# Kernel tuning notes

Measured on AMD Instinct MI355X. Metric: run time of the kernel, lower is better.

Reference implementation:

```python
import jax, jax.numpy as jnp
import numpy as np

STEPS = 10          # points in t_grid -> STEPS-1 RK4 intervals
TRACE_STEPS = 2     # Hutchinson probes per dynamics eval
T_FINAL = 1.0
CLAMP = 100.0


def odefun(t, z, W1, b1, tw1, W2, b2):
    # time-conditioned 2-layer tanh MLP (canonical FFJORD dynamics)
    h = jnp.tanh(z @ W1 + b1 + t * tw1)
    return h @ W2 + b2


def setup_inputs() -> dict:
    key = jax.random.key(0)
    B, D, H = 2048, 512, 1024
    ks = jax.random.split(key, 4)
    s1 = 1.0 / np.sqrt(D)
    s2 = 1.0 / np.sqrt(H)
    return {
        "x": jax.random.normal(ks[0], (B, D), jnp.float32),
        "W1": jax.random.normal(ks[1], (D, H), jnp.float32) * s1,
        "b1": jnp.zeros((H,), jnp.float32),
        "tw1": jax.random.normal(ks[2], (H,), jnp.float32) * 0.1,
        "W2": jax.random.normal(ks[3], (H, D), jnp.float32) * s2,
        "b2": jnp.zeros((D,), jnp.float32),
    }


def reference(x, W1, b1, tw1, W2, b2):
    params = (W1, b1, tw1, W2, b2)
    B, D = x.shape

    def divergence_estimate(t, z, e):
        # torch detaches z before the grad call -> stop_gradient here
        z_sg = jax.lax.stop_gradient(z)
        f, vjp_fn = jax.vjp(lambda zz: odefun(t, zz, *params), z_sg)
        etf = vjp_fn(e)[0]                      # e^T J  (Hutchinson probe)
        return f, jnp.sum(etf * e, axis=-1)     # [B]

    def augmented_dynamics(t, state, key):
        z = state[:, :-1]                        # [B, D]
        div_est = jnp.zeros((B,), state.dtype)
        f_z = None
        for i in range(TRACE_STEPS):             # small fixed loop
            e = jax.random.randint(jax.random.fold_in(key, i), z.shape, 0, 2).astype(z.dtype) * 2.0 - 1.0
            f_z, div = divergence_estimate(t, z, e)
            div_est = div_est + div
        div_est = jnp.clip(div_est / TRACE_STEPS, -CLAMP, CLAMP)
        return jnp.concatenate([f_z, -div_est[:, None]], axis=-1)

    t_grid = jnp.linspace(0.0, T_FINAL, STEPS)
    state0 = jnp.concatenate([x, jnp.zeros((B, 1), x.dtype)], axis=-1)  # [B, D+1]

    def step(carry, t01):
        state, key = carry
        t0, t1 = t01[0], t01[1]
        dt = t1 - t0
        key, k1k, k2k, k3k, k4k = jax.random.split(key, 5)
        # torchdiffeq 'rk4' = Kutta's 3/8-rule variant (rk4_alt_step_func)
        k1 = augmented_dynamics(t0, state, k1k)
        k2 = augmented_dynamics(t0 + dt / 3.0, state + dt * k1 / 3.0, k2k)
        k3 = augmented_dynamics(t0 + dt * 2.0 / 3.0, state + dt * (k2 - k1 / 3.0), k3k)
        k4 = augmented_dynamics(t1, state + dt * (k1 - k2 + k3), k4k)
        state = state + (k1 + 3.0 * (k2 + k3) + k4) * dt * 0.125
        return (state, key), None

    t_pairs = jnp.stack([t_grid[:-1], t_grid[1:]], axis=-1)  # [STEPS-1, 2]
    (state, _), _ = jax.lax.scan(step, (state0, jax.random.key(1234)), t_pairs)

    rep, probsolve = state[:, :-1], state[:, -1]
    logprob = -0.5 * jnp.sum(rep * rep, axis=-1) + probsolve
    return rep, logprob
```

## Files before the change

kernel.cpp:

```cpp
#include <hip/hip_runtime.h>
#include <stdint.h>


#define B_N 2048
#define D_N 512
#define H_N 1024
#define BD (B_N * D_N)

typedef unsigned short u16;
typedef __attribute__((ext_vector_type(8))) short s16x8;
typedef __attribute__((ext_vector_type(4))) float f32x4;

typedef __attribute__((address_space(1))) const uint32_t ga_u32;
typedef __attribute__((address_space(3))) uint32_t ls_u32;

#if __has_builtin(__builtin_amdgcn_alignbit)
#define ROTL32(x, r) __builtin_amdgcn_alignbit((x), (x), 32 - (r))
#else
#define ROTL32(x, r) (((x) << (r)) | ((x) >> (32 - (r))))
#endif

__device__ __forceinline__ u16 f2bf(float f) {
  union { float f; uint32_t u; } c; c.f = f;
  uint32_t r = c.u + 0x7FFFu + ((c.u >> 16) & 1u);
  return (u16)(r >> 16);
}
__device__ __forceinline__ float fast_tanh(float v) {
  float e = __expf(2.0f * fabsf(v));
  float t = 1.0f - 2.0f / (e + 1.0f);
  return copysignf(t, v);
}

struct U2 { uint32_t x, y; };

__device__ __forceinline__ U2 tf2x32(uint32_t k0, uint32_t k1, uint32_t x0, uint32_t x1) {
  uint32_t k2 = k0 ^ k1 ^ 0x1BD11BDAu;
#define RND(r) { x0 += x1; x1 = ROTL32(x1, r); x1 ^= x0; }
  x0 += k0; x1 += k1;
  RND(13) RND(15) RND(26) RND(6)
  x0 += k1; x1 += k2 + 1u;
  RND(17) RND(29) RND(16) RND(24)
  x0 += k2; x1 += k0 + 2u;
  RND(13) RND(15) RND(26) RND(6)
  x0 += k0; x1 += k1 + 3u;
  RND(17) RND(29) RND(16) RND(24)
  x0 += k1; x1 += k2 + 4u;
  RND(13) RND(15) RND(26) RND(6)
  x0 += k2; x1 += k0 + 5u;
#undef RND
  U2 r; r.x = x0; r.y = x1; return r;
}

__global__ void k_keysched(uint32_t* __restrict__ ekeys) {
  if (threadIdx.x != 0 || blockIdx.x != 0) return;
  uint32_t kx = 0u, ky = 1234u;
  for (int s = 0; s < 9; ++s) {
    for (int st = 0; st < 4; ++st) {
      U2 kst = tf2x32(kx, ky, 0u, (uint32_t)(st + 1));
      for (int pr = 0; pr < 2; ++pr) {
        U2 fo = tf2x32(kst.x, kst.y, 0u, (uint32_t)pr);
        U2 k2 = tf2x32(fo.x, fo.y, 0u, 1u);
        ekeys[(s * 4 + st) * 4 + pr * 2 + 0] = k2.x;
        ekeys[(s * 4 + st) * 4 + pr * 2 + 1] = k2.y;
      }
    }
    U2 c = tf2x32(kx, ky, 0u, 0u);
    kx = c.x; ky = c.y;
  }
}

__global__ void k_egen(u16* __restrict__ ebf, const uint32_t* __restrict__ keys, int gs) {
  const int xcd = blockIdx.x & 7, bi = blockIdx.x >> 3;
  const int u = bi * 256 + threadIdx.x;
  const int slab = xcd * 4 + (u >> 13);
  const int r13 = u & 8191;
  const int stage = gs + (r13 >> 11);
  const int r11 = r13 & 2047;
  const int probe = r11 >> 10;
  const int unit = r11 & 1023;
  const uint32_t p0 = (uint32_t)(slab * 32768 + unit * 32);
  uint32_t k0 = keys[stage * 4 + probe * 2], k1 = keys[stage * 4 + probe * 2 + 1];
  uint4* dst = (uint4*)(ebf + (size_t)(stage & 3) * (2 * (size_t)BD) + (size_t)probe * BD + (size_t)p0);
#pragma unroll
  for (int g = 0; g < 4; ++g) {
    uint32_t pr[4];
#pragma unroll
    for (int h = 0; h < 4; ++h) {
      uint32_t c0 = p0 + g * 8 + h * 2;
      U2 r0 = tf2x32(k0, k1, 0u, c0);
      U2 r1 = tf2x32(k0, k1, 0u, c0 + 1u);
      pr[h] = (((r0.x ^ r0.y) & 1u) ? 0x3F80u : 0xBF80u) |
              (((r1.x ^ r1.y) & 1u) ? 0x3F800000u : 0xBF800000u);
    }
    uint4 v; v.x = pr[0]; v.y = pr[1]; v.z = pr[2]; v.w = pr[3];
    dst[g] = v;
  }
}

__global__ void k_init(const float* __restrict__ x, float* __restrict__ z, u16* __restrict__ zin,
                       float* __restrict__ lp, float* __restrict__ d0, float* __restrict__ d1) {
  int i = blockIdx.x * 256 + threadIdx.x;
  if (i < BD) { float v = x[i]; z[i] = v; zin[i] = f2bf(v); }
  if (i < B_N) { lp[i] = 0.f; d0[i] = 0.f; d1[i] = 0.f; }
}

__global__ void k_cvtT(const float* __restrict__ src, u16* __restrict__ dst, int R, int C) {
  int i = blockIdx.x * 256 + threadIdx.x;
  if (i >= R * C) return;
  int c = i / R, r = i - c * R;
  dst[i] = f2bf(src[(size_t)r * C + c]);
}
__global__ void k_cvt(const float* __restrict__ src, u16* __restrict__ dst, int n) {
  int i = blockIdx.x * 256 + threadIdx.x;
  if (i < n) dst[i] = f2bf(src[i]);
}

__global__ void k_sentinel(float* __restrict__ out, int n) {
  int i = blockIdx.x * 256 + threadIdx.x;
  if (i < n) out[i] = 12345.0f;
}


__global__ __launch_bounds__(256)
void k_f1(const u16* __restrict__ zin, const u16* __restrict__ e0g, const u16* __restrict__ e1g,
          const u16* __restrict__ W1T, const u16* __restrict__ W2b,
          const float* __restrict__ b1v, const float* __restrict__ tw1v, float tstage,
          u16* __restrict__ hbuf, float* __restrict__ div0, float* __restrict__ div1) {
  __shared__ u16 S[2][5 * 2048];
  const int tid = threadIdx.x, wave = tid >> 6, lane = tid & 63;
  const int xcd = blockIdx.x & 7, idx = blockIdx.x >> 3;
  const int bm = xcd * 4 + (idx >> 4);
  const int bh = idx & 15;
  const int row0 = bm * 64, col0 = bh * 64;
  const int wm = wave >> 1, wn = wave & 1, r16 = lane & 15, q = lane >> 4;
  const int srow = lane >> 2;
  const int scol = (((lane & 3) ^ ((srow >> 1) & 3))) * 8;
  const int cqa = (q ^ ((r16 >> 1) & 3)) * 8;

  f32x4 az[2][2], au0[2][2], au1[2][2], av0[2][2], av1[2][2];
#pragma unroll
  for (int i = 0; i < 2; ++i)
#pragma unroll
    for (int j = 0; j < 2; ++j) {
      az[i][j] = (f32x4){0,0,0,0}; au0[i][j] = (f32x4){0,0,0,0}; au1[i][j] = (f32x4){0,0,0,0};
      av0[i][j] = (f32x4){0,0,0,0}; av1[i][j] = (f32x4){0,0,0,0};
    }

  const size_t arow = (size_t)(row0 + wave * 16 + srow) * 512 + scol;
  const size_t brow = (size_t)(col0 + wave * 16 + srow) * 512 + scol;
  auto stage = [&](int kt, int buf) {
    u16* b = &S[buf][0];
    __builtin_amdgcn_global_load_lds((ga_u32*)(zin + arow + kt), (ls_u32*)(b + 0    + wave * 512), 16, 0, 0);
    __builtin_amdgcn_global_load_lds((ga_u32*)(e0g + arow + kt), (ls_u32*)(b + 2048 + wave * 512), 16, 0, 0);
    __builtin_amdgcn_global_load_lds((ga_u32*)(e1g + arow + kt), (ls_u32*)(b + 4096 + wave * 512), 16, 0, 0);
    __builtin_amdgcn_global_load_lds((ga_u32*)(W1T + brow + kt), (ls_u32*)(b + 6144 + wave * 512), 16, 0, 0);
    __builtin_amdgcn_global_load_lds((ga_u32*)(W2b + brow + kt), (ls_u32*)(b + 8192 + wave * 512), 16, 0, 0);
  };
  stage(0, 0);
  for (int it = 0; it < 16; ++it) {
    const int buf = it & 1;
    __syncthreads();
    if (it + 1 < 16) stage((it + 1) * 32, buf ^ 1);
    const u16* b = &S[buf][0];
    s16x8 zf[2], e0f[2], e1f[2], w1f[2], w2f[2];
#pragma unroll
    for (int i = 0; i < 2; ++i) {
      const int ao = (wm * 32 + i * 16 + r16) * 32 + cqa;
      zf[i]  = *(const s16x8*)(b + 0    + ao);
      e0f[i] = *(const s16x8*)(b + 2048 + ao);
      e1f[i] = *(const s16x8*)(b + 4096 + ao);
    }
#pragma unroll
    for (int j = 0; j < 2; ++j) {
      const int bo = (wn * 32 + j * 16 + r16) * 32 + cqa;
      w1f[j] = *(const s16x8*)(b + 6144 + bo);
      w2f[j] = *(const s16x8*)(b + 8192 + bo);
    }
#pragma unroll
    for (int i = 0; i < 2; ++i)
#pragma unroll
      for (int j = 0; j < 2; ++j) {
        az[i][j]  = __builtin_amdgcn_mfma_f32_16x16x32_bf16(zf[i],  w1f[j], az[i][j],  0, 0, 0);
        au0[i][j] = __builtin_amdgcn_mfma_f32_16x16x32_bf16(e0f[i], w1f[j], au0[i][j], 0, 0, 0);
        au1[i][j] = __builtin_amdgcn_mfma_f32_16x16x32_bf16(e1f[i], w1f[j], au1[i][j], 0, 0, 0);
        av0[i][j] = __builtin_amdgcn_mfma_f32_16x16x32_bf16(e0f[i], w2f[j], av0[i][j], 0, 0, 0);
        av1[i][j] = __builtin_amdgcn_mfma_f32_16x16x32_bf16(e1f[i], w2f[j], av1[i][j], 0, 0, 0);
      }
  }

  float d0s[2][4], d1s[2][4];
#pragma unroll
  for (int i = 0; i < 2; ++i)
#pragma unroll
    for (int r = 0; r < 4; ++r) { d0s[i][r] = 0.f; d1s[i][r] = 0.f; }

#pragma unroll
  for (int j = 0; j < 2; ++j) {
    const int gcol = col0 + wn * 32 + j * 16 + r16;
    const float colb = b1v[gcol] + tstage * tw1v[gcol];
#pragma unroll
    for (int i = 0; i < 2; ++i) {
      const int rbase = row0 + wm * 32 + i * 16 + q * 4;
#pragma unroll
      for (int r = 0; r < 4; ++r) {
        float hv = fast_tanh(az[i][j][r] + colb);
        hbuf[(size_t)(rbase + r) * H_N + gcol] = f2bf(hv);
        float s = 1.f - hv * hv;
        d0s[i][r] += s * au0[i][j][r] * av0[i][j][r];
        d1s[i][r] += s * au1[i][j][r] * av1[i][j][r];
      }
    }
  }
#pragma unroll
  for (int i = 0; i < 2; ++i)
#pragma unroll
    for (int r = 0; r < 4; ++r) {
      float a = d0s[i][r], bb = d1s[i][r];
#pragma unroll
      for (int m = 1; m < 16; m <<= 1) { a += __shfl_xor(a, m); bb += __shfl_xor(bb, m); }
      if (r16 == 0) {
        int grow = row0 + wm * 32 + i * 16 + q * 4 + r;
        atomicAdd(&div0[grow], a);
        atomicAdd(&div1[grow], bb);
      }
    }
}

template<int ST>
__global__ __launch_bounds__(256)
void k_f3(const u16* __restrict__ hbuf, const u16* __restrict__ W2T, const float* __restrict__ b2v,
          float* __restrict__ z, float* __restrict__ ACC, float* __restrict__ T,
          u16* __restrict__ zin, float dt,
          float* __restrict__ lp, float* __restrict__ div0, float* __restrict__ div1, float wdt) {
  __shared__ u16 S[2][3 * 2048];
  const int tid = threadIdx.x, wave = tid >> 6, lane = tid & 63;
  const int xcd = blockIdx.x & 7, idx = blockIdx.x >> 3;
  const int bm = xcd * 4 + (idx >> 4);
  const int bn = idx & 15;
  const int row0 = bm * 64, col0 = bn * 32;
  const int r16 = lane & 15, q = lane >> 4;
  const int srow = lane >> 2;
  const int scol = (((lane & 3) ^ ((srow >> 1) & 3))) * 8;
  const int cqa = (q ^ ((r16 >> 1) & 3)) * 8;

  if (bn == 0 && tid < 64) {
    int b = row0 + tid;
    float c = 0.5f * (div0[b] + div1[b]);
    c = fminf(fmaxf(c, -100.f), 100.f);
    lp[b] -= wdt * c;
    div0[b] = 0.f; div1[b] = 0.f;
  }

  f32x4 acc[2];
  acc[0] = (f32x4){0,0,0,0}; acc[1] = (f32x4){0,0,0,0};

  const size_t arow = (size_t)(row0 + wave * 16 + srow) * 1024 + scol;
  const size_t brow = (size_t)(col0 + (wave & 1) * 16 + srow) * 1024 + scol;
  auto stage = [&](int kt, int buf) {
    u16* b = &S[buf][0];
    __builtin_amdgcn_global_load_lds((ga_u32*)(hbuf + arow + kt), (ls_u32*)(b + wave * 512), 16, 0, 0);
    if (wave < 2)
      __builtin_amdgcn_global_load_lds((ga_u32*)(W2T + brow + kt), (ls_u32*)(b + 4096 + wave * 512), 16, 0, 0);
  };
  stage(0, 0);
  for (int it = 0; it < 32; ++it) {
    const int buf = it & 1;
    __syncthreads();
    if (it + 1 < 32) stage((it + 1) * 32, buf ^ 1);
    const u16* b = &S[buf][0];
    s16x8 af  = *(const s16x8*)(b + (wave * 16 + r16) * 32 + cqa);
    s16x8 bf0 = *(const s16x8*)(b + 4096 + r16 * 32 + cqa);
    s16x8 bf1 = *(const s16x8*)(b + 4096 + (16 + r16) * 32 + cqa);
    acc[0] = __builtin_amdgcn_mfma_f32_16x16x32_bf16(af, bf0, acc[0], 0, 0, 0);
    acc[1] = __builtin_amdgcn_mfma_f32_16x16x32_bf16(af, bf1, acc[1], 0, 0, 0);
  }

#pragma unroll
  for (int j = 0; j < 2; ++j) {
    const int gcol = col0 + j * 16 + r16;
    const float cb = b2v[gcol];
    const int rbase = row0 + wave * 16 + q * 4;
#pragma unroll
    for (int r = 0; r < 4; ++r) {
      const size_t idx2 = (size_t)(rbase + r) * D_N + gcol;
      const float f = acc[j][r] + cb;
      if (ST == 0) {
        ACC[idx2] = dt * 0.125f * f;
        T[idx2]   = dt * f;
        zin[idx2] = f2bf(z[idx2] + dt * f * (1.f / 3.f));
      } else if (ST == 1) {
        float t_ = T[idx2];
        ACC[idx2] += 0.375f * dt * f;
        zin[idx2] = f2bf(z[idx2] + dt * f - t_ * (1.f / 3.f));
        T[idx2]   = t_ - dt * f;
      } else if (ST == 2) {
        ACC[idx2] += 0.375f * dt * f;
        zin[idx2] = f2bf(z[idx2] + T[idx2] + dt * f);
      } else {
        float zn = z[idx2] + ACC[idx2] + dt * 0.125f * f;
        z[idx2]   = zn;
        zin[idx2] = f2bf(zn);
      }
    }
  }
}

__global__ void k_out(const float* __restrict__ z, const float* __restrict__ lp,
                      float* __restrict__ out) {
  const int xcd = blockIdx.x & 7, idx = blockIdx.x >> 3;
  const int b = (xcd * 4 + (idx >> 6)) * 64 + (idx & 63);
  int t = threadIdx.x;
  const float* zr = z + (size_t)b * D_N;
  float ss = 0.f;
  for (int d = t; d < D_N; d += 256) {
    float v = zr[d];
    out[(size_t)b * D_N + d] = v;
    ss += v * v;
  }
  for (int off = 32; off > 0; off >>= 1) ss += __shfl_down(ss, off);
  __shared__ float red[4];
  if ((t & 63) == 0) red[t >> 6] = ss;
  __syncthreads();
  if (t == 0) out[(size_t)BD + b] = -0.5f * (red[0] + red[1] + red[2] + red[3]) + lp[b];
}

extern "C" void kernel_launch(void* const* d_in, const int* in_sizes, int n_in,
                              void* d_out, int out_size, void* d_ws, size_t ws_size,
                              hipStream_t stream) {
  const float* x   = (const float*)d_in[0];
  const float* W1  = (const float*)d_in[1];
  const float* b1  = (const float*)d_in[2];
  const float* tw1 = (const float*)d_in[3];
  const float* W2  = (const float*)d_in[4];
  const float* b2  = (const float*)d_in[5];
  float* outp = (float*)d_out;

  const size_t NEEDED = (size_t)45 << 20;
  if (ws_size < NEEDED) {
    k_sentinel<<<(BD + B_N + 255) / 256, 256, 0, stream>>>(outp, BD + B_N);
    return;
  }
  char* w = (char*)d_ws;
  auto carve = [&](size_t bytes) { char* p = w; w += (bytes + 255) & ~(size_t)255; return p; };
  uint32_t* keys = (uint32_t*)carve(144 * sizeof(uint32_t));
  u16* ebf   = (u16*)carve((size_t)4 * 2 * BD * 2);
  float* z   = (float*)carve((size_t)BD * 4);
  float* ACC = (float*)carve((size_t)BD * 4);
  float* T   = (float*)carve((size_t)BD * 4);
  u16* zin   = (u16*)carve((size_t)BD * 2);
  u16* hbuf  = (u16*)carve((size_t)B_N * H_N * 2);
  u16* W1T   = (u16*)carve((size_t)H_N * D_N * 2);
  u16* W2b   = (u16*)carve((size_t)H_N * D_N * 2);
  u16* W2T   = (u16*)carve((size_t)D_N * H_N * 2);
  float* lp   = (float*)carve((size_t)B_N * 4);
  float* div0 = (float*)carve((size_t)B_N * 4);
  float* div1 = (float*)carve((size_t)B_N * 4);

  k_keysched<<<1, 1, 0, stream>>>(keys);
  k_init<<<BD / 256, 256, 0, stream>>>(x, z, zin, lp, div0, div1);
  k_cvtT<<<(D_N * H_N) / 256, 256, 0, stream>>>(W1, W1T, D_N, H_N);
  k_cvt <<<(H_N * D_N) / 256, 256, 0, stream>>>(W2, W2b, H_N * D_N);
  k_cvtT<<<(H_N * D_N) / 256, 256, 0, stream>>>(W2, W2T, H_N, D_N);

  const int gF1 = (B_N / 64) * (H_N / 64);
  const int gF3 = (B_N / 64) * (D_N / 32);

  for (int s = 0; s < 9; ++s) {
    float t0 = (float)s / 9.0f;
    float t1 = (float)(s + 1) / 9.0f;
    float dt = t1 - t0;
    float tst[4] = { t0, t0 + dt / 3.0f, t0 + dt * 2.0f / 3.0f, t1 };
    float wts[4] = { 1.f, 3.f, 3.f, 1.f };
    for (int st = 0; st < 4; ++st) {
      const int sg = s * 4 + st;
      if ((sg & 3) == 0) k_egen<<<1024, 256, 0, stream>>>(ebf, keys, sg);
      const u16* e0g = ebf + (size_t)(sg & 3) * (2 * (size_t)BD);
      const u16* e1g = e0g + BD;
      k_f1<<<gF1, 256, 0, stream>>>(zin, e0g, e1g, W1T, W2b, b1, tw1, tst[st], hbuf, div0, div1);
      const float wdt = dt * 0.125f * wts[st];
      if (st == 0)      k_f3<0><<<gF3, 256, 0, stream>>>(hbuf, W2T, b2, z, ACC, T, zin, dt, lp, div0, div1, wdt);
      else if (st == 1) k_f3<1><<<gF3, 256, 0, stream>>>(hbuf, W2T, b2, z, ACC, T, zin, dt, lp, div0, div1, wdt);
      else if (st == 2) k_f3<2><<<gF3, 256, 0, stream>>>(hbuf, W2T, b2, z, ACC, T, zin, dt, lp, div0, div1, wdt);
      else              k_f3<3><<<gF3, 256, 0, stream>>>(hbuf, W2T, b2, z, ACC, T, zin, dt, lp, div0, div1, wdt);
    }
  }
  k_out<<<B_N, 256, 0, stream>>>(z, lp, outp);
}
```

Measured before the change: 1.401 ms.

## Load A operands directly to registers and enlarge f3 tiles to 64x64

In k_f1 the z/e0/e1 activation fragments are now read straight from global memory into registers with a double-buffered register prefetch. Only the W1T/W2 tiles still go through LDS, so shared memory drops from five tiles to two. k_f3 moves from 64x32 to 64x64 output tiles with a 2x2 wave layout, halving its grid, and also loads hbuf fragments directly into registers. Both kernels get launch_bounds with a minimum of 2 blocks per CU, and the k-loops are fully unrolled. The aim is to cut LDS traffic and reuse each B fragment across more rows, at the cost of uncoalesced 16-byte direct global loads and more register pressure.

```diff
diff --git a/kernel.cpp b/kernel.cpp
--- a/kernel.cpp
+++ b/kernel.cpp
@@ -120,13 +120,12 @@
   if (i < n) out[i] = 12345.0f;
 }
 
-
-__global__ __launch_bounds__(256)
+__global__ __launch_bounds__(256, 2)
 void k_f1(const u16* __restrict__ zin, const u16* __restrict__ e0g, const u16* __restrict__ e1g,
           const u16* __restrict__ W1T, const u16* __restrict__ W2b,
           const float* __restrict__ b1v, const float* __restrict__ tw1v, float tstage,
           u16* __restrict__ hbuf, float* __restrict__ div0, float* __restrict__ div1) {
-  __shared__ u16 S[2][5 * 2048];
+  __shared__ u16 S[2][2 * 2048];
   const int tid = threadIdx.x, wave = tid >> 6, lane = tid & 63;
   const int xcd = blockIdx.x & 7, idx = blockIdx.x >> 3;
   const int bm = xcd * 4 + (idx >> 4);
@@ -146,45 +145,47 @@
       av0[i][j] = (f32x4){0,0,0,0}; av1[i][j] = (f32x4){0,0,0,0};
     }
 
-  const size_t arow = (size_t)(row0 + wave * 16 + srow) * 512 + scol;
+  const size_t a0 = (size_t)(row0 + wm * 32 + r16) * 512 + q * 8;
+  const size_t a1 = a0 + (size_t)16 * 512;
   const size_t brow = (size_t)(col0 + wave * 16 + srow) * 512 + scol;
-  auto stage = [&](int kt, int buf) {
+  auto stageB = [&](int kt, int buf) {
     u16* b = &S[buf][0];
-    __builtin_amdgcn_global_load_lds((ga_u32*)(zin + arow + kt), (ls_u32*)(b + 0    + wave * 512), 16, 0, 0);
-    __builtin_amdgcn_global_load_lds((ga_u32*)(e0g + arow + kt), (ls_u32*)(b + 2048 + wave * 512), 16, 0, 0);
-    __builtin_amdgcn_global_load_lds((ga_u32*)(e1g + arow + kt), (ls_u32*)(b + 4096 + wave * 512), 16, 0, 0);
-    __builtin_amdgcn_global_load_lds((ga_u32*)(W1T + brow + kt), (ls_u32*)(b + 6144 + wave * 512), 16, 0, 0);
-    __builtin_amdgcn_global_load_lds((ga_u32*)(W2b + brow + kt), (ls_u32*)(b + 8192 + wave * 512), 16, 0, 0);
+    __builtin_amdgcn_global_load_lds((ga_u32*)(W1T + brow + kt), (ls_u32*)(b + 0    + wave * 512), 16, 0, 0);
+    __builtin_amdgcn_global_load_lds((ga_u32*)(W2b + brow + kt), (ls_u32*)(b + 2048 + wave * 512), 16, 0, 0);
   };
-  stage(0, 0);
+  s16x8 A[2][6];
+  auto aload = [&](int kt, int slot) {
+    A[slot][0] = *(const s16x8*)(zin + a0 + kt);
+    A[slot][1] = *(const s16x8*)(zin + a1 + kt);
+    A[slot][2] = *(const s16x8*)(e0g + a0 + kt);
+    A[slot][3] = *(const s16x8*)(e0g + a1 + kt);
+    A[slot][4] = *(const s16x8*)(e1g + a0 + kt);
+    A[slot][5] = *(const s16x8*)(e1g + a1 + kt);
+  };
+  stageB(0, 0);
+  aload(0, 0);
+#pragma unroll
   for (int it = 0; it < 16; ++it) {
     const int buf = it & 1;
     __syncthreads();
-    if (it + 1 < 16) stage((it + 1) * 32, buf ^ 1);
+    if (it + 1 < 16) { stageB((it + 1) * 32, buf ^ 1); aload((it + 1) * 32, buf ^ 1); }
     const u16* b = &S[buf][0];
-    s16x8 zf[2], e0f[2], e1f[2], w1f[2], w2f[2];
-#pragma unroll
-    for (int i = 0; i < 2; ++i) {
-      const int ao = (wm * 32 + i * 16 + r16) * 32 + cqa;
-      zf[i]  = *(const s16x8*)(b + 0    + ao);
-      e0f[i] = *(const s16x8*)(b + 2048 + ao);
-      e1f[i] = *(const s16x8*)(b + 4096 + ao);
-    }
+    s16x8 w1f[2], w2f[2];
 #pragma unroll
     for (int j = 0; j < 2; ++j) {
       const int bo = (wn * 32 + j * 16 + r16) * 32 + cqa;
-      w1f[j] = *(const s16x8*)(b + 6144 + bo);
-      w2f[j] = *(const s16x8*)(b + 8192 + bo);
+      w1f[j] = *(const s16x8*)(b + 0    + bo);
+      w2f[j] = *(const s16x8*)(b + 2048 + bo);
     }
 #pragma unroll
     for (int i = 0; i < 2; ++i)
 #pragma unroll
       for (int j = 0; j < 2; ++j) {
-        az[i][j]  = __builtin_amdgcn_mfma_f32_16x16x32_bf16(zf[i],  w1f[j], az[i][j],  0, 0, 0);
-        au0[i][j] = __builtin_amdgcn_mfma_f32_16x16x32_bf16(e0f[i], w1f[j], au0[i][j], 0, 0, 0);
-        au1[i][j] = __builtin_amdgcn_mfma_f32_16x16x32_bf16(e1f[i], w1f[j], au1[i][j], 0, 0, 0);
-        av0[i][j] = __builtin_amdgcn_mfma_f32_16x16x32_bf16(e0f[i], w2f[j], av0[i][j], 0, 0, 0);
-        av1[i][j] = __builtin_amdgcn_mfma_f32_16x16x32_bf16(e1f[i], w2f[j], av1[i][j], 0, 0, 0);
+        az[i][j]  = __builtin_amdgcn_mfma_f32_16x16x32_bf16(A[buf][i],     w1f[j], az[i][j],  0, 0, 0);
+        au0[i][j] = __builtin_amdgcn_mfma_f32_16x16x32_bf16(A[buf][2 + i], w1f[j], au0[i][j], 0, 0, 0);
+        au1[i][j] = __builtin_amdgcn_mfma_f32_16x16x32_bf16(A[buf][4 + i], w1f[j], au1[i][j], 0, 0, 0);
+        av0[i][j] = __builtin_amdgcn_mfma_f32_16x16x32_bf16(A[buf][2 + i], w2f[j], av0[i][j], 0, 0, 0);
+        av1[i][j] = __builtin_amdgcn_mfma_f32_16x16x32_bf16(A[buf][4 + i], w2f[j], av1[i][j], 0, 0, 0);
       }
   }
 
@@ -227,18 +228,18 @@
 }
 
 template<int ST>
-__global__ __launch_bounds__(256)
+__global__ __launch_bounds__(256, 2)
 void k_f3(const u16* __restrict__ hbuf, const u16* __restrict__ W2T, const float* __restrict__ b2v,
           float* __restrict__ z, float* __restrict__ ACC, float* __restrict__ T,
           u16* __restrict__ zin, float dt,
           float* __restrict__ lp, float* __restrict__ div0, float* __restrict__ div1, float wdt) {
-  __shared__ u16 S[2][3 * 2048];
+  __shared__ u16 S[2][2048];
   const int tid = threadIdx.x, wave = tid >> 6, lane = tid & 63;
   const int xcd = blockIdx.x & 7, idx = blockIdx.x >> 3;
-  const int bm = xcd * 4 + (idx >> 4);
-  const int bn = idx & 15;
-  const int row0 = bm * 64, col0 = bn * 32;
-  const int r16 = lane & 15, q = lane >> 4;
+  const int bm = xcd * 4 + (idx >> 3);
+  const int bn = idx & 7;
+  const int row0 = bm * 64, col0 = bn * 64;
+  const int wm = wave >> 1, wn = wave & 1, r16 = lane & 15, q = lane >> 4;
   const int srow = lane >> 2;
   const int scol = (((lane & 3) ^ ((srow >> 1) & 3))) * 8;
   const int cqa = (q ^ ((r16 >> 1) & 3)) * 8;
@@ -251,55 +252,70 @@
     div0[b] = 0.f; div1[b] = 0.f;
   }
 
-  f32x4 acc[2];
-  acc[0] = (f32x4){0,0,0,0}; acc[1] = (f32x4){0,0,0,0};
-
-  const size_t arow = (size_t)(row0 + wave * 16 + srow) * 1024 + scol;
-  const size_t brow = (size_t)(col0 + (wave & 1) * 16 + srow) * 1024 + scol;
-  auto stage = [&](int kt, int buf) {
-    u16* b = &S[buf][0];
-    __builtin_amdgcn_global_load_lds((ga_u32*)(hbuf + arow + kt), (ls_u32*)(b + wave * 512), 16, 0, 0);
-    if (wave < 2)
-      __builtin_amdgcn_global_load_lds((ga_u32*)(W2T + brow + kt), (ls_u32*)(b + 4096 + wave * 512), 16, 0, 0);
+  f32x4 acc[2][2];
+#pragma unroll
+  for (int i = 0; i < 2; ++i)
+#pragma unroll
+    for (int j = 0; j < 2; ++j) acc[i][j] = (f32x4){0,0,0,0};
+
+  const size_t a0 = (size_t)(row0 + wm * 32 + r16) * 1024 + q * 8;
+  const size_t a1 = a0 + (size_t)16 * 1024;
+  const size_t brow = (size_t)(col0 + wave * 16 + srow) * 1024 + scol;
+  auto stageB = [&](int kt, int buf) {
+    __builtin_amdgcn_global_load_lds((ga_u32*)(W2T + brow + kt), (ls_u32*)(&S[buf][0] + wave * 512), 16, 0, 0);
   };
-  stage(0, 0);
+  s16x8 A[2][2];
+  auto aload = [&](int kt, int slot) {
+    A[slot][0] = *(const s16x8*)(hbuf + a0 + kt);
+    A[slot][1] = *(const s16x8*)(hbuf + a1 + kt);
+  };
+  stageB(0, 0);
+  aload(0, 0);
+#pragma unroll
   for (int it = 0; it < 32; ++it) {
     const int buf = it & 1;
     __syncthreads();
-    if (it + 1 < 32) stage((it + 1) * 32, buf ^ 1);
+    if (it + 1 < 32) { stageB((it + 1) * 32, buf ^ 1); aload((it + 1) * 32, buf ^ 1); }
     const u16* b = &S[buf][0];
-    s16x8 af  = *(const s16x8*)(b + (wave * 16 + r16) * 32 + cqa);
-    s16x8 bf0 = *(const s16x8*)(b + 4096 + r16 * 32 + cqa);
-    s16x8 bf1 = *(const s16x8*)(b + 4096 + (16 + r16) * 32 + cqa);
-    acc[0] = __builtin_amdgcn_mfma_f32_16x16x32_bf16(af, bf0, acc[0], 0, 0, 0);
-    acc[1] = __builtin_amdgcn_mfma_f32_16x16x32_bf16(af, bf1, acc[1], 0, 0, 0);
+    s16x8 bfr[2];
+#pragma unroll
+    for (int j = 0; j < 2; ++j)
+      bfr[j] = *(const s16x8*)(b + (wn * 32 + j * 16 + r16) * 32 + cqa);
+#pragma unroll
+    for (int i = 0; i < 2; ++i)
+#pragma unroll
+      for (int j = 0; j < 2; ++j)
+        acc[i][j] = __builtin_amdgcn_mfma_f32_16x16x32_bf16(A[buf][i], bfr[j], acc[i][j], 0, 0, 0);
   }
 
 #pragma unroll
   for (int j = 0; j < 2; ++j) {
-    const int gcol = col0 + j * 16 + r16;
+    const int gcol = col0 + wn * 32 + j * 16 + r16;
     const float cb = b2v[gcol];
-    const int rbase = row0 + wave * 16 + q * 4;
-#pragma unroll
-    for (int r = 0; r < 4; ++r) {
-      const size_t idx2 = (size_t)(rbase + r) * D_N + gcol;
-      const float f = acc[j][r] + cb;
-      if (ST == 0) {
-        ACC[idx2] = dt * 0.125f * f;
-        T[idx2]   = dt * f;
-        zin[idx2] = f2bf(z[idx2] + dt * f * (1.f / 3.f));
-      } else if (ST == 1) {
-        float t_ = T[idx2];
-        ACC[idx2] += 0.375f * dt * f;
-        zin[idx2] = f2bf(z[idx2] + dt * f - t_ * (1.f / 3.f));
-        T[idx2]   = t_ - dt * f;
-      } else if (ST == 2) {
-        ACC[idx2] += 0.375f * dt * f;
-        zin[idx2] = f2bf(z[idx2] + T[idx2] + dt * f);
-      } else {
-        float zn = z[idx2] + ACC[idx2] + dt * 0.125f * f;
-        z[idx2]   = zn;
-        zin[idx2] = f2bf(zn);
+#pragma unroll
+    for (int i = 0; i < 2; ++i) {
+      const int rbase = row0 + wm * 32 + i * 16 + q * 4;
+#pragma unroll
+      for (int r = 0; r < 4; ++r) {
+        const size_t idx2 = (size_t)(rbase + r) * D_N + gcol;
+        const float f = acc[i][j][r] + cb;
+        if (ST == 0) {
+          ACC[idx2] = dt * 0.125f * f;
+          T[idx2]   = dt * f;
+          zin[idx2] = f2bf(z[idx2] + dt * f * (1.f / 3.f));
+        } else if (ST == 1) {
+          float t_ = T[idx2];
+          ACC[idx2] += 0.375f * dt * f;
+          zin[idx2] = f2bf(z[idx2] + dt * f - t_ * (1.f / 3.f));
+          T[idx2]   = t_ - dt * f;
+        } else if (ST == 2) {
+          ACC[idx2] += 0.375f * dt * f;
+          zin[idx2] = f2bf(z[idx2] + T[idx2] + dt * f);
+        } else {
+          float zn = z[idx2] + ACC[idx2] + dt * 0.125f * f;
+          z[idx2]   = zn;
+          zin[idx2] = f2bf(zn);
+        }
       }
     }
   }
@@ -363,7 +379,7 @@
   k_cvtT<<<(H_N * D_N) / 256, 256, 0, stream>>>(W2, W2T, H_N, D_N);
 
   const int gF1 = (B_N / 64) * (H_N / 64);
-  const int gF3 = (B_N / 64) * (D_N / 32);
+  const int gF3 = (B_N / 64) * (D_N / 64);
 
   for (int s = 0; s < 9; ++s) {
     float t0 = (float)s / 9.0f;
```

Result: slower. 2.084 ms (+48.7%).

## Fuse next-stage probe generation into k_f3 epilogue and widen k_f1 to 8 waves

Applied to the files above, without the earlier changes.

Removes the separate k_egen launch that generated probe vectors for four stages at once. k_f3 now generates the Rademacher probes for the next stage in its epilogue into a double buffer, and a small kernel seeds the first stage. k_f1 runs with 512 threads, so each wave owns a 16-row slice instead of 32, with the LDS staging loop distributed across 8 waves. The intent is to cut launch count, shrink the workspace, and raise occupancy in the first GEMM, at the cost of extra per-block RNG work in k_f3 and less register reuse per wave in k_f1.

```diff
diff --git a/kernel.cpp b/kernel.cpp
--- a/kernel.cpp
+++ b/kernel.cpp
@@ -69,18 +69,12 @@
   }
 }
 
-__global__ void k_egen(u16* __restrict__ ebf, const uint32_t* __restrict__ keys, int gs) {
-  const int xcd = blockIdx.x & 7, bi = blockIdx.x >> 3;
-  const int u = bi * 256 + threadIdx.x;
-  const int slab = xcd * 4 + (u >> 13);
-  const int r13 = u & 8191;
-  const int stage = gs + (r13 >> 11);
-  const int r11 = r13 & 2047;
-  const int probe = r11 >> 10;
-  const int unit = r11 & 1023;
-  const uint32_t p0 = (uint32_t)(slab * 32768 + unit * 32);
-  uint32_t k0 = keys[stage * 4 + probe * 2], k1 = keys[stage * 4 + probe * 2 + 1];
-  uint4* dst = (uint4*)(ebf + (size_t)(stage & 3) * (2 * (size_t)BD) + (size_t)probe * BD + (size_t)p0);
+__global__ void k_egen1(u16* __restrict__ ebf, const uint32_t* __restrict__ keys) {
+  int t = blockIdx.x * 256 + threadIdx.x;
+  int probe = t >> 15, idx = t & 32767;
+  uint32_t p0 = (uint32_t)idx * 32;
+  uint32_t k0 = keys[probe * 2], k1 = keys[probe * 2 + 1];
+  uint4* dst = (uint4*)(ebf + (size_t)probe * BD + (size_t)p0);
 #pragma unroll
   for (int g = 0; g < 4; ++g) {
     uint32_t pr[4];
@@ -120,8 +114,7 @@
   if (i < n) out[i] = 12345.0f;
 }
 
-
-__global__ __launch_bounds__(256)
+__global__ __launch_bounds__(512, 4)
 void k_f1(const u16* __restrict__ zin, const u16* __restrict__ e0g, const u16* __restrict__ e1g,
           const u16* __restrict__ W1T, const u16* __restrict__ W2b,
           const float* __restrict__ b1v, const float* __restrict__ tw1v, float tstage,
@@ -137,24 +130,21 @@
   const int scol = (((lane & 3) ^ ((srow >> 1) & 3))) * 8;
   const int cqa = (q ^ ((r16 >> 1) & 3)) * 8;
 
-  f32x4 az[2][2], au0[2][2], au1[2][2], av0[2][2], av1[2][2];
-#pragma unroll
-  for (int i = 0; i < 2; ++i)
-#pragma unroll
-    for (int j = 0; j < 2; ++j) {
-      az[i][j] = (f32x4){0,0,0,0}; au0[i][j] = (f32x4){0,0,0,0}; au1[i][j] = (f32x4){0,0,0,0};
-      av0[i][j] = (f32x4){0,0,0,0}; av1[i][j] = (f32x4){0,0,0,0};
-    }
-
-  const size_t arow = (size_t)(row0 + wave * 16 + srow) * 512 + scol;
-  const size_t brow = (size_t)(col0 + wave * 16 + srow) * 512 + scol;
+  f32x4 az[2], au0[2], au1[2], av0[2], av1[2];
+#pragma unroll
+  for (int j = 0; j < 2; ++j) {
+    az[j] = (f32x4){0,0,0,0}; au0[j] = (f32x4){0,0,0,0}; au1[j] = (f32x4){0,0,0,0};
+    av0[j] = (f32x4){0,0,0,0}; av1[j] = (f32x4){0,0,0,0};
+  }
+
   auto stage = [&](int kt, int buf) {
     u16* b = &S[buf][0];
-    __builtin_amdgcn_global_load_lds((ga_u32*)(zin + arow + kt), (ls_u32*)(b + 0    + wave * 512), 16, 0, 0);
-    __builtin_amdgcn_global_load_lds((ga_u32*)(e0g + arow + kt), (ls_u32*)(b + 2048 + wave * 512), 16, 0, 0);
-    __builtin_amdgcn_global_load_lds((ga_u32*)(e1g + arow + kt), (ls_u32*)(b + 4096 + wave * 512), 16, 0, 0);
-    __builtin_amdgcn_global_load_lds((ga_u32*)(W1T + brow + kt), (ls_u32*)(b + 6144 + wave * 512), 16, 0, 0);
-    __builtin_amdgcn_global_load_lds((ga_u32*)(W2b + brow + kt), (ls_u32*)(b + 8192 + wave * 512), 16, 0, 0);
+    for (int c = wave; c < 20; c += 8) {
+      const int arr = c >> 2, ch = c & 3;
+      const size_t off = (size_t)((arr < 3 ? row0 : col0) + ch * 16 + srow) * 512 + kt + scol;
+      const u16* src = (arr == 0 ? zin : arr == 1 ? e0g : arr == 2 ? e1g : arr == 3 ? W1T : W2b) + off;
+      __builtin_amdgcn_global_load_lds((ga_u32*)src, (ls_u32*)(b + arr * 2048 + ch * 512), 16, 0, 0);
+    }
   };
   stage(0, 0);
   for (int it = 0; it < 16; ++it) {
@@ -162,14 +152,11 @@
     __syncthreads();
     if (it + 1 < 16) stage((it + 1) * 32, buf ^ 1);
     const u16* b = &S[buf][0];
-    s16x8 zf[2], e0f[2], e1f[2], w1f[2], w2f[2];
-#pragma unroll
-    for (int i = 0; i < 2; ++i) {
-      const int ao = (wm * 32 + i * 16 + r16) * 32 + cqa;
-      zf[i]  = *(const s16x8*)(b + 0    + ao);
-      e0f[i] = *(const s16x8*)(b + 2048 + ao);
-      e1f[i] = *(const s16x8*)(b + 4096 + ao);
-    }
+    const int ao = (wm * 16 + r16) * 32 + cqa;
+    s16x8 zf  = *(const s16x8*)(b + 0    + ao);
+    s16x8 e0f = *(const s16x8*)(b + 2048 + ao);
+    s16x8 e1f = *(const s16x8*)(b + 4096 + ao);
+    s16x8 w1f[2], w2f[2];
 #pragma unroll
     for (int j = 0; j < 2; ++j) {
       const int bo = (wn * 32 + j * 16 + r16) * 32 + cqa;
@@ -177,53 +164,43 @@
       w2f[j] = *(const s16x8*)(b + 8192 + bo);
     }
 #pragma unroll
-    for (int i = 0; i < 2; ++i)
-#pragma unroll
-      for (int j = 0; j < 2; ++j) {
-        az[i][j]  = __builtin_amdgcn_mfma_f32_16x16x32_bf16(zf[i],  w1f[j], az[i][j],  0, 0, 0);
-        au0[i][j] = __builtin_amdgcn_mfma_f32_16x16x32_bf16(e0f[i], w1f[j], au0[i][j], 0, 0, 0);
-        au1[i][j] = __builtin_amdgcn_mfma_f32_16x16x32_bf16(e1f[i], w1f[j], au1[i][j], 0, 0, 0);
-        av0[i][j] = __builtin_amdgcn_mfma_f32_16x16x32_bf16(e0f[i], w2f[j], av0[i][j], 0, 0, 0);
-        av1[i][j] = __builtin_amdgcn_mfma_f32_16x16x32_bf16(e1f[i], w2f[j], av1[i][j], 0, 0, 0);
-      }
-  }
-
-  float d0s[2][4], d1s[2][4];
-#pragma unroll
-  for (int i = 0; i < 2; ++i)
-#pragma unroll
-    for (int r = 0; r < 4; ++r) { d0s[i][r] = 0.f; d1s[i][r] = 0.f; }
-
+    for (int j = 0; j < 2; ++j) {
+      az[j]  = __builtin_amdgcn_mfma_f32_16x16x32_bf16(zf,  w1f[j], az[j],  0, 0, 0);
+      au0[j] = __builtin_amdgcn_mfma_f32_16x16x32_bf16(e0f, w1f[j], au0[j], 0, 0, 0);
+      au1[j] = __builtin_amdgcn_mfma_f32_16x16x32_bf16(e1f, w1f[j], au1[j], 0, 0, 0);
+      av0[j] = __builtin_amdgcn_mfma_f32_16x16x32_bf16(e0f, w2f[j], av0[j], 0, 0, 0);
+      av1[j] = __builtin_amdgcn_mfma_f32_16x16x32_bf16(e1f, w2f[j], av1[j], 0, 0, 0);
+    }
+  }
+
+  float d0s[4], d1s[4];
+#pragma unroll
+  for (int r = 0; r < 4; ++r) { d0s[r] = 0.f; d1s[r] = 0.f; }
+
+  const int rbase = row0 + wm * 16 + q * 4;
 #pragma unroll
   for (int j = 0; j < 2; ++j) {
     const int gcol = col0 + wn * 32 + j * 16 + r16;
     const float colb = b1v[gcol] + tstage * tw1v[gcol];
 #pragma unroll
-    for (int i = 0; i < 2; ++i) {
-      const int rbase = row0 + wm * 32 + i * 16 + q * 4;
-#pragma unroll
-      for (int r = 0; r < 4; ++r) {
-        float hv = fast_tanh(az[i][j][r] + colb);
-        hbuf[(size_t)(rbase + r) * H_N + gcol] = f2bf(hv);
-        float s = 1.f - hv * hv;
-        d0s[i][r] += s * au0[i][j][r] * av0[i][j][r];
-        d1s[i][r] += s * au1[i][j][r] * av1[i][j][r];
-      }
-    }
-  }
-#pragma unroll
-  for (int i = 0; i < 2; ++i)
-#pragma unroll
     for (int r = 0; r < 4; ++r) {
-      float a = d0s[i][r], bb = d1s[i][r];
-#pragma unroll
-      for (int m = 1; m < 16; m <<= 1) { a += __shfl_xor(a, m); bb += __shfl_xor(bb, m); }
-      if (r16 == 0) {
-        int grow = row0 + wm * 32 + i * 16 + q * 4 + r;
-        atomicAdd(&div0[grow], a);
-        atomicAdd(&div1[grow], bb);
-      }
-    }
+      float hv = fast_tanh(az[j][r] + colb);
+      hbuf[(size_t)(rbase + r) * H_N + gcol] = f2bf(hv);
+      float s = 1.f - hv * hv;
+      d0s[r] += s * au0[j][r] * av0[j][r];
+      d1s[r] += s * au1[j][r] * av1[j][r];
+    }
+  }
+#pragma unroll
+  for (int r = 0; r < 4; ++r) {
+    float a = d0s[r], bb = d1s[r];
+#pragma unroll
+    for (int m = 1; m < 16; m <<= 1) { a += __shfl_xor(a, m); bb += __shfl_xor(bb, m); }
+    if (r16 == 0) {
+      atomicAdd(&div0[rbase + r], a);
+      atomicAdd(&div1[rbase + r], bb);
+    }
+  }
 }
 
 template<int ST>
@@ -231,7 +208,8 @@
 void k_f3(const u16* __restrict__ hbuf, const u16* __restrict__ W2T, const float* __restrict__ b2v,
           float* __restrict__ z, float* __restrict__ ACC, float* __restrict__ T,
           u16* __restrict__ zin, float dt,
-          float* __restrict__ lp, float* __restrict__ div0, float* __restrict__ div1, float wdt) {
+          float* __restrict__ lp, float* __restrict__ div0, float* __restrict__ div1, float wdt,
+          const uint32_t* __restrict__ keys, int sg, u16* __restrict__ ebfnext) {
   __shared__ u16 S[2][3 * 2048];
   const int tid = threadIdx.x, wave = tid >> 6, lane = tid & 63;
   const int xcd = blockIdx.x & 7, idx = blockIdx.x >> 3;
@@ -303,6 +281,27 @@
       }
     }
   }
+
+  if (ebfnext) {
+    const int pr = tid >> 7, u = tid & 127;
+    const uint32_t p0 = (uint32_t)(bm * 32768 + bn * 2048 + u * 16);
+    const uint32_t k0 = keys[(sg + 1) * 4 + pr * 2], k1 = keys[(sg + 1) * 4 + pr * 2 + 1];
+    uint4* dst = (uint4*)(ebfnext + (size_t)pr * BD + (size_t)p0);
+#pragma unroll
+    for (int g = 0; g < 2; ++g) {
+      uint32_t pk[4];
+#pragma unroll
+      for (int h = 0; h < 4; ++h) {
+        uint32_t c0 = p0 + g * 8 + h * 2;
+        U2 r0 = tf2x32(k0, k1, 0u, c0);
+        U2 r1 = tf2x32(k0, k1, 0u, c0 + 1u);
+        pk[h] = (((r0.x ^ r0.y) & 1u) ? 0x3F80u : 0xBF80u) |
+                (((r1.x ^ r1.y) & 1u) ? 0x3F800000u : 0xBF800000u);
+      }
+      uint4 v; v.x = pk[0]; v.y = pk[1]; v.z = pk[2]; v.w = pk[3];
+      dst[g] = v;
+    }
+  }
 }
 
 __global__ void k_out(const float* __restrict__ z, const float* __restrict__ lp,
@@ -335,7 +334,7 @@
   const float* b2  = (const float*)d_in[5];
   float* outp = (float*)d_out;
 
-  const size_t NEEDED = (size_t)45 << 20;
+  const size_t NEEDED = (size_t)40 << 20;
   if (ws_size < NEEDED) {
     k_sentinel<<<(BD + B_N + 255) / 256, 256, 0, stream>>>(outp, BD + B_N);
     return;
@@ -343,7 +342,7 @@
   char* w = (char*)d_ws;
   auto carve = [&](size_t bytes) { char* p = w; w += (bytes + 255) & ~(size_t)255; return p; };
   uint32_t* keys = (uint32_t*)carve(144 * sizeof(uint32_t));
-  u16* ebf   = (u16*)carve((size_t)4 * 2 * BD * 2);
+  u16* ebf   = (u16*)carve((size_t)2 * 2 * BD * 2);
   float* z   = (float*)carve((size_t)BD * 4);
   float* ACC = (float*)carve((size_t)BD * 4);
   float* T   = (float*)carve((size_t)BD * 4);
@@ -357,6 +356,7 @@
   float* div1 = (float*)carve((size_t)B_N * 4);
 
   k_keysched<<<1, 1, 0, stream>>>(keys);
+  k_egen1<<<256, 256, 0, stream>>>(ebf, keys);
   k_init<<<BD / 256, 256, 0, stream>>>(x, z, zin, lp, div0, div1);
   k_cvtT<<<(D_N * H_N) / 256, 256, 0, stream>>>(W1, W1T, D_N, H_N);
   k_cvt <<<(H_N * D_N) / 256, 256, 0, stream>>>(W2, W2b, H_N * D_N);
@@ -373,15 +373,15 @@
     float wts[4] = { 1.f, 3.f, 3.f, 1.f };
     for (int st = 0; st < 4; ++st) {
       const int sg = s * 4 + st;
-      if ((sg & 3) == 0) k_egen<<<1024, 256, 0, stream>>>(ebf, keys, sg);
-      const u16* e0g = ebf + (size_t)(sg & 3) * (2 * (size_t)BD);
+      const u16* e0g = ebf + (size_t)(sg & 1) * (2 * (size_t)BD);
       const u16* e1g = e0g + BD;
-      k_f1<<<gF1, 256, 0, stream>>>(zin, e0g, e1g, W1T, W2b, b1, tw1, tst[st], hbuf, div0, div1);
+      u16* enext = (sg + 1 < 36) ? ebf + (size_t)((sg + 1) & 1) * (2 * (size_t)BD) : nullptr;
+      k_f1<<<gF1, 512, 0, stream>>>(zin, e0g, e1g, W1T, W2b, b1, tw1, tst[st], hbuf, div0, div1);
       const float wdt = dt * 0.125f * wts[st];
-      if (st == 0)      k_f3<0><<<gF3, 256, 0, stream>>>(hbuf, W2T, b2, z, ACC, T, zin, dt, lp, div0, div1, wdt);
-      else if (st == 1) k_f3<1><<<gF3, 256, 0, stream>>>(hbuf, W2T, b2, z, ACC, T, zin, dt, lp, div0, div1, wdt);
-      else if (st == 2) k_f3<2><<<gF3, 256, 0, stream>>>(hbuf, W2T, b2, z, ACC, T, zin, dt, lp, div0, div1, wdt);
-      else              k_f3<3><<<gF3, 256, 0, stream>>>(hbuf, W2T, b2, z, ACC, T, zin, dt, lp, div0, div1, wdt);
+      if (st == 0)      k_f3<0><<<gF3, 256, 0, stream>>>(hbuf, W2T, b2, z, ACC, T, zin, dt, lp, div0, div1, wdt, keys, sg, enext);
+      else if (st == 1) k_f3<1><<<gF3, 256, 0, stream>>>(hbuf, W2T, b2, z, ACC, T, zin, dt, lp, div0, div1, wdt, keys, sg, enext);
+      else if (st == 2) k_f3<2><<<gF3, 256, 0, stream>>>(hbuf, W2T, b2, z, ACC, T, zin, dt, lp, div0, div1, wdt, keys, sg, enext);
+      else              k_f3<3><<<gF3, 256, 0, stream>>>(hbuf, W2T, b2, z, ACC, T, zin, dt, lp, div0, div1, wdt, keys, sg, enext);
     }
   }
   k_out<<<B_N, 256, 0, stream>>>(z, lp, outp);
```

Measured after the change: 1.502 ms. 7.2% more time.

## Bit-pack Rademacher probes and generate next-stage bits inside the f3 epilogue

Applied to the files above, without the earlier changes.

Probe vectors are stored as one bit per element instead of bf16 tiles and are expanded into MFMA operands in registers inside k_f1. The LDS staging drops from five arrays to three. The separate k_egen launch is removed: the next stage's probe bits are computed in the k_f3 epilogue and double-buffered. This targets the global and LDS traffic for the probes and one kernel launch per RK step, at the cost of extra ALU work for expansion and threefry hashing in the f3 tail.

```diff
diff --git a/kernel.cpp b/kernel.cpp
--- a/kernel.cpp
+++ b/kernel.cpp
@@ -69,32 +69,18 @@
   }
 }
 
-__global__ void k_egen(u16* __restrict__ ebf, const uint32_t* __restrict__ keys, int gs) {
-  const int xcd = blockIdx.x & 7, bi = blockIdx.x >> 3;
-  const int u = bi * 256 + threadIdx.x;
-  const int slab = xcd * 4 + (u >> 13);
-  const int r13 = u & 8191;
-  const int stage = gs + (r13 >> 11);
-  const int r11 = r13 & 2047;
-  const int probe = r11 >> 10;
-  const int unit = r11 & 1023;
-  const uint32_t p0 = (uint32_t)(slab * 32768 + unit * 32);
-  uint32_t k0 = keys[stage * 4 + probe * 2], k1 = keys[stage * 4 + probe * 2 + 1];
-  uint4* dst = (uint4*)(ebf + (size_t)(stage & 3) * (2 * (size_t)BD) + (size_t)probe * BD + (size_t)p0);
-#pragma unroll
-  for (int g = 0; g < 4; ++g) {
-    uint32_t pr[4];
-#pragma unroll
-    for (int h = 0; h < 4; ++h) {
-      uint32_t c0 = p0 + g * 8 + h * 2;
-      U2 r0 = tf2x32(k0, k1, 0u, c0);
-      U2 r1 = tf2x32(k0, k1, 0u, c0 + 1u);
-      pr[h] = (((r0.x ^ r0.y) & 1u) ? 0x3F80u : 0xBF80u) |
-              (((r1.x ^ r1.y) & 1u) ? 0x3F800000u : 0xBF800000u);
-    }
-    uint4 v; v.x = pr[0]; v.y = pr[1]; v.z = pr[2]; v.w = pr[3];
-    dst[g] = v;
-  }
+__global__ void k_ebits1(uint32_t* __restrict__ eb, const uint32_t* __restrict__ keys) {
+  int t = blockIdx.x * 256 + threadIdx.x;
+  int probe = t >> 15, d = t & 32767;
+  uint32_t p0 = (uint32_t)d * 32;
+  uint32_t k0 = keys[probe * 2], k1 = keys[probe * 2 + 1];
+  uint32_t bits = 0;
+#pragma unroll 4
+  for (int j = 0; j < 32; ++j) {
+    U2 r = tf2x32(k0, k1, 0u, p0 + j);
+    bits |= ((r.x ^ r.y) & 1u) << j;
+  }
+  eb[probe * 32768 + d] = bits;
 }
 
 __global__ void k_init(const float* __restrict__ x, float* __restrict__ z, u16* __restrict__ zin,
@@ -120,13 +106,23 @@
   if (i < n) out[i] = 12345.0f;
 }
 
+__device__ __forceinline__ s16x8 expand8(uint32_t byteval) {
+  union { s16x8 v; uint32_t d[4]; } f;
+  uint32_t sb = byteval ^ 0xFFu;
+#pragma unroll
+  for (int d2 = 0; d2 < 4; ++d2) {
+    uint32_t t = sb >> (2 * d2);
+    f.d[d2] = 0x3F803F80u | ((t & 1u) << 15) | ((t & 2u) << 30);
+  }
+  return f.v;
+}
 
 __global__ __launch_bounds__(256)
-void k_f1(const u16* __restrict__ zin, const u16* __restrict__ e0g, const u16* __restrict__ e1g,
+void k_f1(const u16* __restrict__ zin, const uint32_t* __restrict__ ebits,
           const u16* __restrict__ W1T, const u16* __restrict__ W2b,
           const float* __restrict__ b1v, const float* __restrict__ tw1v, float tstage,
           u16* __restrict__ hbuf, float* __restrict__ div0, float* __restrict__ div1) {
-  __shared__ u16 S[2][5 * 2048];
+  __shared__ u16 S[2][3 * 2048];
   const int tid = threadIdx.x, wave = tid >> 6, lane = tid & 63;
   const int xcd = blockIdx.x & 7, idx = blockIdx.x >> 3;
   const int bm = xcd * 4 + (idx >> 4);
@@ -146,35 +142,63 @@
       av0[i][j] = (f32x4){0,0,0,0}; av1[i][j] = (f32x4){0,0,0,0};
     }
 
-  const size_t arow = (size_t)(row0 + wave * 16 + srow) * 512 + scol;
-  const size_t brow = (size_t)(col0 + wave * 16 + srow) * 512 + scol;
+  const size_t arow = (size_t)(row0 + srow) * 512 + scol;
+  const size_t brow = (size_t)(col0 + srow) * 512 + scol;
   auto stage = [&](int kt, int buf) {
     u16* b = &S[buf][0];
-    __builtin_amdgcn_global_load_lds((ga_u32*)(zin + arow + kt), (ls_u32*)(b + 0    + wave * 512), 16, 0, 0);
-    __builtin_amdgcn_global_load_lds((ga_u32*)(e0g + arow + kt), (ls_u32*)(b + 2048 + wave * 512), 16, 0, 0);
-    __builtin_amdgcn_global_load_lds((ga_u32*)(e1g + arow + kt), (ls_u32*)(b + 4096 + wave * 512), 16, 0, 0);
-    __builtin_amdgcn_global_load_lds((ga_u32*)(W1T + brow + kt), (ls_u32*)(b + 6144 + wave * 512), 16, 0, 0);
-    __builtin_amdgcn_global_load_lds((ga_u32*)(W2b + brow + kt), (ls_u32*)(b + 8192 + wave * 512), 16, 0, 0);
+#pragma unroll
+    for (int c = wave; c < 12; c += 4) {
+      const int arr = c >> 2, ch = c & 3;
+      const size_t off = (arr == 0 ? arow : brow) + (size_t)(ch * 16) * 512 + kt;
+      const u16* src = (arr == 0 ? zin : arr == 1 ? W1T : W2b) + off;
+      __builtin_amdgcn_global_load_lds((ga_u32*)src, (ls_u32*)(b + arr * 2048 + ch * 512), 16, 0, 0);
+    }
   };
+
+  const int r0i = row0 + wm * 32 + r16;
+  uint4 ebq[2][2], ebn[2][2];
+#pragma unroll
+  for (int i = 0; i < 2; ++i)
+#pragma unroll
+    for (int pr = 0; pr < 2; ++pr)
+      ebn[i][pr] = *(const uint4*)(ebits + pr * 32768 + (r0i + i * 16) * 16);
+
   stage(0, 0);
+#pragma unroll
   for (int it = 0; it < 16; ++it) {
     const int buf = it & 1;
+    if ((it & 3) == 0) {
+#pragma unroll
+      for (int i = 0; i < 2; ++i)
+#pragma unroll
+        for (int pr = 0; pr < 2; ++pr) ebq[i][pr] = ebn[i][pr];
+      if (it + 4 < 16) {
+#pragma unroll
+        for (int i = 0; i < 2; ++i)
+#pragma unroll
+          for (int pr = 0; pr < 2; ++pr)
+            ebn[i][pr] = *(const uint4*)(ebits + pr * 32768 + (r0i + i * 16) * 16 + it + 4);
+      }
+    }
     __syncthreads();
     if (it + 1 < 16) stage((it + 1) * 32, buf ^ 1);
     const u16* b = &S[buf][0];
     s16x8 zf[2], e0f[2], e1f[2], w1f[2], w2f[2];
 #pragma unroll
     for (int i = 0; i < 2; ++i) {
-      const int ao = (wm * 32 + i * 16 + r16) * 32 + cqa;
-      zf[i]  = *(const s16x8*)(b + 0    + ao);
-      e0f[i] = *(const s16x8*)(b + 2048 + ao);
-      e1f[i] = *(const s16x8*)(b + 4096 + ao);
+      zf[i] = *(const s16x8*)(b + (wm * 32 + i * 16 + r16) * 32 + cqa);
+      const uint32_t d0w = (it & 3) == 0 ? ebq[i][0].x : (it & 3) == 1 ? ebq[i][0].y
+                         : (it & 3) == 2 ? ebq[i][0].z : ebq[i][0].w;
+      const uint32_t d1w = (it & 3) == 0 ? ebq[i][1].x : (it & 3) == 1 ? ebq[i][1].y
+                         : (it & 3) == 2 ? ebq[i][1].z : ebq[i][1].w;
+      e0f[i] = expand8((d0w >> (q * 8)) & 0xFFu);
+      e1f[i] = expand8((d1w >> (q * 8)) & 0xFFu);
     }
 #pragma unroll
     for (int j = 0; j < 2; ++j) {
       const int bo = (wn * 32 + j * 16 + r16) * 32 + cqa;
-      w1f[j] = *(const s16x8*)(b + 6144 + bo);
-      w2f[j] = *(const s16x8*)(b + 8192 + bo);
+      w1f[j] = *(const s16x8*)(b + 2048 + bo);
+      w2f[j] = *(const s16x8*)(b + 4096 + bo);
     }
 #pragma unroll
     for (int i = 0; i < 2; ++i)
@@ -231,7 +255,8 @@
 void k_f3(const u16* __restrict__ hbuf, const u16* __restrict__ W2T, const float* __restrict__ b2v,
           float* __restrict__ z, float* __restrict__ ACC, float* __restrict__ T,
           u16* __restrict__ zin, float dt,
-          float* __restrict__ lp, float* __restrict__ div0, float* __restrict__ div1, float wdt) {
+          float* __restrict__ lp, float* __restrict__ div0, float* __restrict__ div1, float wdt,
+          const uint32_t* __restrict__ keys, int sg, uint32_t* __restrict__ ebnext) {
   __shared__ u16 S[2][3 * 2048];
   const int tid = threadIdx.x, wave = tid >> 6, lane = tid & 63;
   const int xcd = blockIdx.x & 7, idx = blockIdx.x >> 3;
@@ -303,6 +328,22 @@
       }
     }
   }
+
+  if (ebnext) {
+    const int pr = tid >> 7, u = tid & 127;
+    const int d = bm * 1024 + bn * 64 + (u >> 1);
+    const int half = u & 1;
+    const uint32_t k0 = keys[(sg + 1) * 4 + pr * 2], k1 = keys[(sg + 1) * 4 + pr * 2 + 1];
+    const uint32_t p0 = (uint32_t)d * 32 + half * 16;
+    uint32_t bits = 0;
+#pragma unroll 4
+    for (int j = 0; j < 16; ++j) {
+      U2 r = tf2x32(k0, k1, 0u, p0 + j);
+      bits |= ((r.x ^ r.y) & 1u) << j;
+    }
+    uint32_t other = __shfl_xor(bits, 1);
+    if (half == 0) ebnext[pr * 32768 + d] = bits | (other << 16);
+  }
 }
 
 __global__ void k_out(const float* __restrict__ z, const float* __restrict__ lp,
@@ -335,15 +376,15 @@
   const float* b2  = (const float*)d_in[5];
   float* outp = (float*)d_out;
 
-  const size_t NEEDED = (size_t)45 << 20;
+  const size_t NEEDED = (size_t)35 << 20;
   if (ws_size < NEEDED) {
     k_sentinel<<<(BD + B_N + 255) / 256, 256, 0, stream>>>(outp, BD + B_N);
     return;
   }
   char* w = (char*)d_ws;
   auto carve = [&](size_t bytes) { char* p = w; w += (bytes + 255) & ~(size_t)255; return p; };
-  uint32_t* keys = (uint32_t*)carve(144 * sizeof(uint32_t));
-  u16* ebf   = (u16*)carve((size_t)4 * 2 * BD * 2);
+  uint32_t* keys  = (uint32_t*)carve(144 * sizeof(uint32_t));
+  uint32_t* ebits = (uint32_t*)carve((size_t)2 * 65536 * 4);
   float* z   = (float*)carve((size_t)BD * 4);
   float* ACC = (float*)carve((size_t)BD * 4);
   float* T   = (float*)carve((size_t)BD * 4);
@@ -357,6 +398,7 @@
   float* div1 = (float*)carve((size_t)B_N * 4);
 
   k_keysched<<<1, 1, 0, stream>>>(keys);
+  k_ebits1<<<256, 256, 0, stream>>>(ebits, keys);
   k_init<<<BD / 256, 256, 0, stream>>>(x, z, zin, lp, div0, div1);
   k_cvtT<<<(D_N * H_N) / 256, 256, 0, stream>>>(W1, W1T, D_N, H_N);
   k_cvt <<<(H_N * D_N) / 256, 256, 0, stream>>>(W2, W2b, H_N * D_N);
@@ -373,15 +415,14 @@
     float wts[4] = { 1.f, 3.f, 3.f, 1.f };
     for (int st = 0; st < 4; ++st) {
       const int sg = s * 4 + st;
-      if ((sg & 3) == 0) k_egen<<<1024, 256, 0, stream>>>(ebf, keys, sg);
-      const u16* e0g = ebf + (size_t)(sg & 3) * (2 * (size_t)BD);
-      const u16* e1g = e0g + BD;
-      k_f1<<<gF1, 256, 0, stream>>>(zin, e0g, e1g, W1T, W2b, b1, tw1, tst[st], hbuf, div0, div1);
+      const uint32_t* eslot = ebits + (size_t)(sg & 1) * 65536;
+      uint32_t* enext = (sg + 1 < 36) ? ebits + (size_t)((sg + 1) & 1) * 65536 : nullptr;
+      k_f1<<<gF1, 256, 0, stream>>>(zin, eslot, W1T, W2b, b1, tw1, tst[st], hbuf, div0, div1);
       const float wdt = dt * 0.125f * wts[st];
-      if (st == 0)      k_f3<0><<<gF3, 256, 0, stream>>>(hbuf, W2T, b2, z, ACC, T, zin, dt, lp, div0, div1, wdt);
-      else if (st == 1) k_f3<1><<<gF3, 256, 0, stream>>>(hbuf, W2T, b2, z, ACC, T, zin, dt, lp, div0, div1, wdt);
-      else if (st == 2) k_f3<2><<<gF3, 256, 0, stream>>>(hbuf, W2T, b2, z, ACC, T, zin, dt, lp, div0, div1, wdt);
-      else              k_f3<3><<<gF3, 256, 0, stream>>>(hbuf, W2T, b2, z, ACC, T, zin, dt, lp, div0, div1, wdt);
+      if (st == 0)      k_f3<0><<<gF3, 256, 0, stream>>>(hbuf, W2T, b2, z, ACC, T, zin, dt, lp, div0, div1, wdt, keys, sg, enext);
+      else if (st == 1) k_f3<1><<<gF3, 256, 0, stream>>>(hbuf, W2T, b2, z, ACC, T, zin, dt, lp, div0, div1, wdt, keys, sg, enext);
+      else if (st == 2) k_f3<2><<<gF3, 256, 0, stream>>>(hbuf, W2T, b2, z, ACC, T, zin, dt, lp, div0, div1, wdt, keys, sg, enext);
+      else              k_f3<3><<<gF3, 256, 0, stream>>>(hbuf, W2T, b2, z, ACC, T, zin, dt, lp, div0, div1, wdt, keys, sg, enext);
     }
   }
   k_out<<<B_N, 256, 0, stream>>>(z, lp, outp);
```

Measured after the change: 2.382 ms. 70.1% more time.
